# Kernel optimization log

Measured on AMD Instinct MI355X. Metric: run time of the kernel, lower is better.

## Reference

```python
import jax, jax.numpy as jnp
import numpy as np

NUM_AGENTS = 1000
N_ACTIONS = 16
HIDDEN = 256
COMM_STEPS = 4
B, M = 1024, 64


def setup_inputs() -> dict:
    key = jax.random.key(0)
    ks = jax.random.split(key, 8)
    agent_ids = jax.random.randint(ks[0], (B, M), 0, NUM_AGENTS)
    emb = jax.random.normal(ks[1], (NUM_AGENTS, HIDDEN), dtype=jnp.float32) * 0.1
    s1 = 1.0 / np.sqrt(3 * HIDDEN)
    W1 = jax.random.uniform(ks[2], (3 * HIDDEN, HIDDEN), jnp.float32, -s1, s1)
    b1 = jax.random.uniform(ks[3], (HIDDEN,), jnp.float32, -s1, s1)
    s2 = 1.0 / np.sqrt(HIDDEN)
    W2 = jax.random.uniform(ks[4], (HIDDEN, HIDDEN), jnp.float32, -s2, s2)
    b2 = jax.random.uniform(ks[5], (HIDDEN,), jnp.float32, -s2, s2)
    Wd = jax.random.uniform(ks[6], (HIDDEN, N_ACTIONS), jnp.float32, -s2, s2)
    bd = jax.random.uniform(ks[7], (N_ACTIONS,), jnp.float32, -s2, s2)
    return {"agent_ids": agent_ids, "emb": emb, "W1": W1, "b1": b1,
            "W2": W2, "b2": b2, "Wd": Wd, "bd": bd}


def reference(agent_ids, emb, W1, b1, W2, b2, Wd, bd):
    # h0: (B, M, H) embedding lookup
    h0 = emb[agent_ids]
    h = h0
    m = agent_ids.shape[1]
    inv = 1.0 / (m - 1)
    for _ in range(COMM_STEPS):
        # mean of other agents' hidden states: c_j = (sum_k h_k - h_j)/(M-1)
        c = (jnp.sum(h, axis=1, keepdims=True) - h) * inv
        x = jnp.concatenate([h, c, h0], axis=-1)  # (B, M, 3H)
        delta = jax.nn.relu(jnp.einsum('bmi,ih->bmh', x, W1) + b1)
        delta = jnp.einsum('bmi,ih->bmh', delta, W2) + b2
        h = h + delta  # residual (use_skip=True)
    logits = jnp.einsum('bmh,ha->bma', h, Wd) + bd
    return logits
```

## Files before the change

kernel.cpp:

```cpp
#include <hip/hip_runtime.h>

#define HID 256
#define NB 1024
#define NACT 16
#define HSTRIDE 528

typedef __bf16 bf16x8 __attribute__((ext_vector_type(8)));
typedef float  f32x4  __attribute__((ext_vector_type(4)));

#define HA_LO   33792
#define S_OFF   67584
#define LDS_TOT 68608

#define PREP_N (4 * 65536 + 4096)

__device__ __forceinline__ unsigned short f2bf(float x) {
    union { __bf16 b; unsigned short u; } v; v.b = (__bf16)x; return v.u;
}
__device__ __forceinline__ float bf2f(unsigned short u) {
    union { unsigned short u; __bf16 b; } v; v.u = u; return (float)v.b;
}
__device__ __forceinline__ float b2f_lo(unsigned v) { return bf2f((unsigned short)(v & 0xffffu)); }
__device__ __forceinline__ float b2f_hi(unsigned v) { return bf2f((unsigned short)(v >> 16)); }
__device__ __forceinline__ unsigned pack2(float a, float b) {
    return (unsigned)f2bf(a) | ((unsigned)f2bf(b) << 16);
}

__global__ __launch_bounds__(256) void prep_k(const float* __restrict__ W1,
                                              const float* __restrict__ W2,
                                              const float* __restrict__ Wd,
                                              unsigned short* __restrict__ WAh, unsigned short* __restrict__ WAl,
                                              unsigned short* __restrict__ WHh, unsigned short* __restrict__ WHl,
                                              unsigned short* __restrict__ WBh, unsigned short* __restrict__ WBl,
                                              unsigned short* __restrict__ WCh, unsigned short* __restrict__ WCl,
                                              unsigned short* __restrict__ WDh, unsigned short* __restrict__ WDl) {
    int i = blockIdx.x * 256 + threadIdx.x;
    const float inv = 1.0f / 63.0f;
    if (i < 4 * 65536) {
        int mat = i >> 16, j = i & 65535;
        int kq = j >> 13, r = j & 8191;
        int nb = r >> 9, r2 = r & 511;
        int l = r2 >> 3, e = r2 & 7;
        int n = nb * 16 + (l & 15);
        int k = kq * 32 + (l >> 4) * 8 + e;
        float val;
        if (mat == 0)      val = W1[k * 256 + n] - inv * W1[(256 + k) * 256 + n];
        else if (mat == 1) val = W1[(512 + k) * 256 + n];
        else if (mat == 2) val = W2[k * 256 + n];
        else               val = inv * W1[(256 + k) * 256 + n];
        unsigned short hi = f2bf(val);
        unsigned short lo = f2bf(val - bf2f(hi));
        if (mat == 0)      { WAh[j] = hi; WAl[j] = lo; }
        else if (mat == 1) { WHh[j] = hi; WHl[j] = lo; }
        else if (mat == 2) { WBh[j] = hi; WBl[j] = lo; }
        else               { WCh[j] = hi; WCl[j] = lo; }
    } else if (i < PREP_N) {
        int j = i - 4 * 65536, a = j >> 8, k = j & 255;
        float val = Wd[k * 16 + a];
        unsigned short hi = f2bf(val);
        WDh[j] = hi; WDl[j] = f2bf(val - bf2f(hi));
    }
}

__device__ __forceinline__ void kloopL2(const unsigned short* __restrict__ Wfh,
                                        const unsigned short* __restrict__ Wfl,
                                        const char* hA, f32x4 (&acc)[4][2],
                                        size_t lbase, int l15, int g)
{
    #pragma unroll 2
    for (int kq = 0; kq < 8; ++kq) {
        const int cb = g * 128 + kq * 16;
        bf16x8 ah[4], al[4];
        #pragma unroll
        for (int mt = 0; mt < 4; ++mt) {
            int rb = (mt * 16 + l15) * HSTRIDE;
            ah[mt] = *(const bf16x8*)(hA + rb + cb);
            al[mt] = *(const bf16x8*)(hA + HA_LO + rb + cb);
        }
        const size_t kb = (size_t)kq * 8192 + lbase;
        #pragma unroll
        for (int nt = 0; nt < 2; ++nt) {
            bf16x8 bh = *(const bf16x8*)(Wfh + kb + nt * 512);
            bf16x8 bl = *(const bf16x8*)(Wfl + kb + nt * 512);
            #pragma unroll
            for (int mt = 0; mt < 4; ++mt) {
                acc[mt][nt] = __builtin_amdgcn_mfma_f32_16x16x32_bf16(bh, ah[mt], acc[mt][nt], 0, 0, 0);
                acc[mt][nt] = __builtin_amdgcn_mfma_f32_16x16x32_bf16(bh, al[mt], acc[mt][nt], 0, 0, 0);
                acc[mt][nt] = __builtin_amdgcn_mfma_f32_16x16x32_bf16(bl, ah[mt], acc[mt][nt], 0, 0, 0);
            }
        }
    }
}

__global__ __launch_bounds__(512, 2) void fused_all(
    const int* __restrict__ ids, const float* __restrict__ emb,
    const unsigned short* __restrict__ WAh, const unsigned short* __restrict__ WAl,
    const unsigned short* __restrict__ WHh, const unsigned short* __restrict__ WHl,
    const unsigned short* __restrict__ WBh, const unsigned short* __restrict__ WBl,
    const unsigned short* __restrict__ WCh, const unsigned short* __restrict__ WCl,
    const unsigned short* __restrict__ WDh, const unsigned short* __restrict__ WDl,
    const float* __restrict__ b1, const float* __restrict__ b2,
    const float* __restrict__ bd, float* __restrict__ out)
{
    __shared__ __align__(16) char lds[LDS_TOT];
    const int tid = threadIdx.x;
    const int lane = tid & 63;
    const int w = tid >> 6;
    const int l15 = lane & 15, g = lane >> 4;
    const size_t rowbase = (size_t)blockIdx.x * 64;
    char* hA = lds;
    float* Sf = (float*)(lds + S_OFF);
    const size_t lbase = ((size_t)(w * 2) * 64 + lane) * 8;
    const int cb0 = w * 32 + g * 4;

    int colb[2];
    #pragma unroll
    for (int nt = 0; nt < 2; ++nt) {
        int o = w * 4 + nt * 2 + (g >> 1);
        colb[nt] = ((o & 3) * 8 + (o >> 2)) * 16 + (g & 1) * 8;
    }

    {
        int r = tid >> 3, c0q = tid & 7;
        const float4* src = (const float4*)(emb + (size_t)ids[rowbase + r] * HID + c0q * 32);
        char* dh = hA + r * HSTRIDE;
        #pragma unroll
        for (int j = 0; j < 8; ++j) {
            float4 v = src[j];
            unsigned short h0 = f2bf(v.x), h1 = f2bf(v.y), h2 = f2bf(v.z), h3 = f2bf(v.w);
            unsigned short q0 = f2bf(v.x - bf2f(h0)), q1 = f2bf(v.y - bf2f(h1)),
                           q2 = f2bf(v.z - bf2f(h2)), q3 = f2bf(v.w - bf2f(h3));
            int byte = (j >> 1) * 128 + c0q * 16 + (j & 1) * 8;
            *(uint2*)(dh + byte) = make_uint2((unsigned)h0 | ((unsigned)h1 << 16),
                                              (unsigned)h2 | ((unsigned)h3 << 16));
            *(uint2*)(dh + HA_LO + byte) = make_uint2((unsigned)q0 | ((unsigned)q1 << 16),
                                                      (unsigned)q2 | ((unsigned)q3 << 16));
        }
    }
    __syncthreads();

    if (tid < 256) {
        int cperm = (((tid >> 3) & 3) * 8 + (tid >> 5)) * 16 + (tid & 7) * 2;
        float ssum = 0.f;
        #pragma unroll 8
        for (int m = 0; m < 64; ++m) {
            int byte = m * HSTRIDE + cperm;
            ssum += bf2f(*(const unsigned short*)(hA + byte))
                  + bf2f(*(const unsigned short*)(hA + HA_LO + byte));
        }
        Sf[tid] = ssum;
    }
    __syncthreads();

    f32x4 acc[4][2], u0r[4][2];
    #pragma unroll
    for (int mt = 0; mt < 4; ++mt)
        #pragma unroll
        for (int nt = 0; nt < 2; ++nt) acc[mt][nt] = (f32x4){0.f, 0.f, 0.f, 0.f};

    kloopL2(WHh, WHl, hA, acc, lbase, l15, g);
    #pragma unroll
    for (int nt = 0; nt < 2; ++nt) {
        f32x4 b1v = *(const f32x4*)(b1 + cb0 + nt * 16);
        #pragma unroll
        for (int mt = 0; mt < 4; ++mt)
            u0r[mt][nt] = acc[mt][nt] + b1v;
    }

    for (int s = 0; s < 4; ++s) {
        f32x4 tacc[2];
        tacc[0] = tacc[1] = (f32x4){0.f, 0.f, 0.f, 0.f};
        #pragma unroll 2
        for (int kq = 0; kq < 8; ++kq) {
            const float* sp = Sf + kq * 32 + g * 8;
            f32x4 sa = *(const f32x4*)sp;
            f32x4 sb = *(const f32x4*)(sp + 4);
            unsigned sh[4], sl[4];
            sh[0] = pack2(sa[0], sa[1]); sh[1] = pack2(sa[2], sa[3]);
            sh[2] = pack2(sb[0], sb[1]); sh[3] = pack2(sb[2], sb[3]);
            sl[0] = pack2(sa[0] - b2f_lo(sh[0]), sa[1] - b2f_hi(sh[0]));
            sl[1] = pack2(sa[2] - b2f_lo(sh[1]), sa[3] - b2f_hi(sh[1]));
            sl[2] = pack2(sb[0] - b2f_lo(sh[2]), sb[1] - b2f_hi(sh[2]));
            sl[3] = pack2(sb[2] - b2f_lo(sh[3]), sb[3] - b2f_hi(sh[3]));
            bf16x8 shv = *(const bf16x8*)sh;
            bf16x8 slv = *(const bf16x8*)sl;
            const size_t kb = (size_t)kq * 8192 + lbase;
            #pragma unroll
            for (int nt = 0; nt < 2; ++nt) {
                bf16x8 wch = *(const bf16x8*)(WCh + kb + nt * 512);
                bf16x8 wcl = *(const bf16x8*)(WCl + kb + nt * 512);
                tacc[nt] = __builtin_amdgcn_mfma_f32_16x16x32_bf16(wch, shv, tacc[nt], 0, 0, 0);
                tacc[nt] = __builtin_amdgcn_mfma_f32_16x16x32_bf16(wch, slv, tacc[nt], 0, 0, 0);
                tacc[nt] = __builtin_amdgcn_mfma_f32_16x16x32_bf16(wcl, shv, tacc[nt], 0, 0, 0);
            }
        }

        #pragma unroll
        for (int mt = 0; mt < 4; ++mt)
            #pragma unroll
            for (int nt = 0; nt < 2; ++nt)
                acc[mt][nt] = u0r[mt][nt] + tacc[nt];
        kloopL2(WAh, WAl, hA, acc, lbase, l15, g);

        __syncthreads();
        #pragma unroll
        for (int mt = 0; mt < 4; ++mt)
            #pragma unroll
            for (int nt = 0; nt < 2; ++nt) {
                f32x4 b2v = *(const f32x4*)(b2 + cb0 + nt * 16);
                int byte = (mt * 16 + l15) * HSTRIDE + colb[nt];
                uint2 ph = *(const uint2*)(hA + byte);
                uint2 pl = *(const uint2*)(hA + HA_LO + byte);
                f32x4 hres;
                hres[0] = b2f_lo(ph.x) + b2f_lo(pl.x);
                hres[1] = b2f_hi(ph.x) + b2f_hi(pl.x);
                hres[2] = b2f_lo(ph.y) + b2f_lo(pl.y);
                hres[3] = b2f_hi(ph.y) + b2f_hi(pl.y);
                f32x4 av = acc[mt][nt];
                float a0 = fmaxf(av[0], 0.f), a1 = fmaxf(av[1], 0.f);
                float a2 = fmaxf(av[2], 0.f), a3 = fmaxf(av[3], 0.f);
                unsigned h01 = pack2(a0, a1), h23 = pack2(a2, a3);
                float r0 = a0 - b2f_lo(h01);
                float r1 = a1 - b2f_hi(h01);
                float r2 = a2 - b2f_lo(h23);
                float r3 = a3 - b2f_hi(h23);
                *(uint2*)(hA + byte) = make_uint2(h01, h23);
                *(uint2*)(hA + HA_LO + byte) = make_uint2(pack2(r0, r1), pack2(r2, r3));
                acc[mt][nt] = hres + b2v;
            }
        __syncthreads();

        kloopL2(WBh, WBl, hA, acc, lbase, l15, g);

        __syncthreads();
        #pragma unroll
        for (int mt = 0; mt < 4; ++mt)
            #pragma unroll
            for (int nt = 0; nt < 2; ++nt) {
                int byte = (mt * 16 + l15) * HSTRIDE + colb[nt];
                f32x4 av = acc[mt][nt];
                unsigned h01 = pack2(av[0], av[1]), h23 = pack2(av[2], av[3]);
                float r0 = av[0] - b2f_lo(h01);
                float r1 = av[1] - b2f_hi(h01);
                float r2 = av[2] - b2f_lo(h23);
                float r3 = av[3] - b2f_hi(h23);
                *(uint2*)(hA + byte) = make_uint2(h01, h23);
                *(uint2*)(hA + HA_LO + byte) = make_uint2(pack2(r0, r1), pack2(r2, r3));
            }
        if (s < 3) {
            #pragma unroll
            for (int nt = 0; nt < 2; ++nt) {
                f32x4 cs = (acc[0][nt] + acc[1][nt]) + (acc[2][nt] + acc[3][nt]);
                #pragma unroll
                for (int d = 1; d < 16; d <<= 1) {
                    cs[0] += __shfl_xor(cs[0], d);
                    cs[1] += __shfl_xor(cs[1], d);
                    cs[2] += __shfl_xor(cs[2], d);
                    cs[3] += __shfl_xor(cs[3], d);
                }
                if (l15 == 0) *(f32x4*)(Sf + cb0 + nt * 16) = cs;
            }
        }
        __syncthreads();
    }

    if (w < 4) {
        f32x4 dacc = (f32x4){0.f, 0.f, 0.f, 0.f};
        #pragma unroll 2
        for (int kq = 0; kq < 8; ++kq) {
            int byte = (w * 16 + l15) * HSTRIDE + g * 128 + kq * 16;
            bf16x8 hh = *(const bf16x8*)(hA + byte);
            bf16x8 hl = *(const bf16x8*)(hA + HA_LO + byte);
            const int k = kq * 32;
            bf16x8 wdh = *(const bf16x8*)(WDh + (size_t)l15 * 256 + k + g * 8);
            bf16x8 wdl = *(const bf16x8*)(WDl + (size_t)l15 * 256 + k + g * 8);
            dacc = __builtin_amdgcn_mfma_f32_16x16x32_bf16(wdh, hh, dacc, 0, 0, 0);
            dacc = __builtin_amdgcn_mfma_f32_16x16x32_bf16(wdh, hl, dacc, 0, 0, 0);
            dacc = __builtin_amdgcn_mfma_f32_16x16x32_bf16(wdl, hh, dacc, 0, 0, 0);
        }
        f32x4 bdv = *(const f32x4*)(bd + g * 4);
        f32x4 o = dacc + bdv;
        *(f32x4*)(out + (rowbase + w * 16 + l15) * NACT + g * 4) = o;
    }
}

extern "C" void kernel_launch(void* const* d_in, const int* in_sizes, int n_in,
                              void* d_out, int out_size, void* d_ws, size_t ws_size,
                              hipStream_t stream) {
    const int*   ids = (const int*)d_in[0];
    const float* emb = (const float*)d_in[1];
    const float* W1  = (const float*)d_in[2];
    const float* b1  = (const float*)d_in[3];
    const float* W2  = (const float*)d_in[4];
    const float* b2  = (const float*)d_in[5];
    const float* Wd  = (const float*)d_in[6];
    const float* bd  = (const float*)d_in[7];
    float* out = (float*)d_out;

    char* p = (char*)d_ws;
    unsigned short* WAh = (unsigned short*)p; p += 65536 * 2;
    unsigned short* WAl = (unsigned short*)p; p += 65536 * 2;
    unsigned short* WHh = (unsigned short*)p; p += 65536 * 2;
    unsigned short* WHl = (unsigned short*)p; p += 65536 * 2;
    unsigned short* WBh = (unsigned short*)p; p += 65536 * 2;
    unsigned short* WBl = (unsigned short*)p; p += 65536 * 2;
    unsigned short* WCh = (unsigned short*)p; p += 65536 * 2;
    unsigned short* WCl = (unsigned short*)p; p += 65536 * 2;
    unsigned short* WDh = (unsigned short*)p; p += 4096 * 2;
    unsigned short* WDl = (unsigned short*)p; p += 4096 * 2;

    prep_k<<<(PREP_N + 255) / 256, 256, 0, stream>>>(W1, W2, Wd, WAh, WAl, WHh, WHl,
                                                     WBh, WBl, WCh, WCl, WDh, WDl);
    fused_all<<<NB, 512, 0, stream>>>(ids, emb, WAh, WAl, WHh, WHl, WBh, WBl,
                                      WCh, WCl, WDh, WDl, b1, b2, bd, out);
}
```

Measured before the change: 278.4 us.

## Spill per-row h0 projection to global scratch and simplify LDS column layout

Moves the precomputed h0·W1 projection plus bias (u0r, 32 floats per lane) out of registers into a global workspace buffer, reloading it each communication step. The aim is to free VGPRs so the kernel can hold its launch bounds without spilling and improve occupancy. It also replaces the permuted column layout in LDS with a plain linear layout and changes the k-loop addressing to match. The cost is extra global memory traffic per step, and the new LDS access pattern may cause different bank conflicts.

Measured after the change: 352.5 us. 1.27x slower.

```diff
diff --git a/kernel.cpp b/kernel.cpp
--- a/kernel.cpp
+++ b/kernel.cpp
@@ -69,7 +69,7 @@
 {
     #pragma unroll 2
     for (int kq = 0; kq < 8; ++kq) {
-        const int cb = g * 128 + kq * 16;
+        const int cb = kq * 64 + g * 16;
         bf16x8 ah[4], al[4];
         #pragma unroll
         for (int mt = 0; mt < 4; ++mt) {
@@ -99,6 +99,7 @@
     const unsigned short* __restrict__ WBh, const unsigned short* __restrict__ WBl,
     const unsigned short* __restrict__ WCh, const unsigned short* __restrict__ WCl,
     const unsigned short* __restrict__ WDh, const unsigned short* __restrict__ WDl,
+    float* __restrict__ U0,
     const float* __restrict__ b1, const float* __restrict__ b2,
     const float* __restrict__ bd, float* __restrict__ out)
 {
@@ -112,39 +113,31 @@
     float* Sf = (float*)(lds + S_OFF);
     const size_t lbase = ((size_t)(w * 2) * 64 + lane) * 8;
     const int cb0 = w * 32 + g * 4;
-
-    int colb[2];
-    #pragma unroll
-    for (int nt = 0; nt < 2; ++nt) {
-        int o = w * 4 + nt * 2 + (g >> 1);
-        colb[nt] = ((o & 3) * 8 + (o >> 2)) * 16 + (g & 1) * 8;
-    }
+    f32x4* u0p = (f32x4*)U0 + (((size_t)blockIdx.x * 8 + w) * 8) * 64 + lane;
 
     {
-        int r = tid >> 3, c0q = tid & 7;
-        const float4* src = (const float4*)(emb + (size_t)ids[rowbase + r] * HID + c0q * 32);
-        char* dh = hA + r * HSTRIDE;
+        int r = tid >> 3, c0 = (tid & 7) * 32;
+        const float4* src = (const float4*)(emb + (size_t)ids[rowbase + r] * HID + c0);
+        char* dh = hA + r * HSTRIDE + c0 * 2;
         #pragma unroll
         for (int j = 0; j < 8; ++j) {
             float4 v = src[j];
             unsigned short h0 = f2bf(v.x), h1 = f2bf(v.y), h2 = f2bf(v.z), h3 = f2bf(v.w);
             unsigned short q0 = f2bf(v.x - bf2f(h0)), q1 = f2bf(v.y - bf2f(h1)),
                            q2 = f2bf(v.z - bf2f(h2)), q3 = f2bf(v.w - bf2f(h3));
-            int byte = (j >> 1) * 128 + c0q * 16 + (j & 1) * 8;
-            *(uint2*)(dh + byte) = make_uint2((unsigned)h0 | ((unsigned)h1 << 16),
-                                              (unsigned)h2 | ((unsigned)h3 << 16));
-            *(uint2*)(dh + HA_LO + byte) = make_uint2((unsigned)q0 | ((unsigned)q1 << 16),
-                                                      (unsigned)q2 | ((unsigned)q3 << 16));
+            *(uint2*)(dh + j * 8) = make_uint2((unsigned)h0 | ((unsigned)h1 << 16),
+                                               (unsigned)h2 | ((unsigned)h3 << 16));
+            *(uint2*)(dh + HA_LO + j * 8) = make_uint2((unsigned)q0 | ((unsigned)q1 << 16),
+                                                       (unsigned)q2 | ((unsigned)q3 << 16));
         }
     }
     __syncthreads();
 
     if (tid < 256) {
-        int cperm = (((tid >> 3) & 3) * 8 + (tid >> 5)) * 16 + (tid & 7) * 2;
         float ssum = 0.f;
         #pragma unroll 8
         for (int m = 0; m < 64; ++m) {
-            int byte = m * HSTRIDE + cperm;
+            int byte = m * HSTRIDE + tid * 2;
             ssum += bf2f(*(const unsigned short*)(hA + byte))
                   + bf2f(*(const unsigned short*)(hA + HA_LO + byte));
         }
@@ -152,7 +145,7 @@
     }
     __syncthreads();
 
-    f32x4 acc[4][2], u0r[4][2];
+    f32x4 acc[4][2];
     #pragma unroll
     for (int mt = 0; mt < 4; ++mt)
         #pragma unroll
@@ -163,8 +156,10 @@
     for (int nt = 0; nt < 2; ++nt) {
         f32x4 b1v = *(const f32x4*)(b1 + cb0 + nt * 16);
         #pragma unroll
-        for (int mt = 0; mt < 4; ++mt)
-            u0r[mt][nt] = acc[mt][nt] + b1v;
+        for (int mt = 0; mt < 4; ++mt) {
+            u0p[(mt * 2 + nt) * 64] = acc[mt][nt] + b1v;
+            acc[mt][nt] = (f32x4){0.f, 0.f, 0.f, 0.f};
+        }
     }
 
     for (int s = 0; s < 4; ++s) {
@@ -199,7 +194,7 @@
         for (int mt = 0; mt < 4; ++mt)
             #pragma unroll
             for (int nt = 0; nt < 2; ++nt)
-                acc[mt][nt] = u0r[mt][nt] + tacc[nt];
+                acc[mt][nt] = u0p[(mt * 2 + nt) * 64] + tacc[nt];
         kloopL2(WAh, WAl, hA, acc, lbase, l15, g);
 
         __syncthreads();
@@ -208,7 +203,7 @@
             #pragma unroll
             for (int nt = 0; nt < 2; ++nt) {
                 f32x4 b2v = *(const f32x4*)(b2 + cb0 + nt * 16);
-                int byte = (mt * 16 + l15) * HSTRIDE + colb[nt];
+                int byte = (mt * 16 + l15) * HSTRIDE + (cb0 + nt * 16) * 2;
                 uint2 ph = *(const uint2*)(hA + byte);
                 uint2 pl = *(const uint2*)(hA + HA_LO + byte);
                 f32x4 hres;
@@ -237,7 +232,7 @@
         for (int mt = 0; mt < 4; ++mt)
             #pragma unroll
             for (int nt = 0; nt < 2; ++nt) {
-                int byte = (mt * 16 + l15) * HSTRIDE + colb[nt];
+                int byte = (mt * 16 + l15) * HSTRIDE + (cb0 + nt * 16) * 2;
                 f32x4 av = acc[mt][nt];
                 unsigned h01 = pack2(av[0], av[1]), h23 = pack2(av[2], av[3]);
                 float r0 = av[0] - b2f_lo(h01);
@@ -268,7 +263,7 @@
         f32x4 dacc = (f32x4){0.f, 0.f, 0.f, 0.f};
         #pragma unroll 2
         for (int kq = 0; kq < 8; ++kq) {
-            int byte = (w * 16 + l15) * HSTRIDE + g * 128 + kq * 16;
+            int byte = (w * 16 + l15) * HSTRIDE + kq * 64 + g * 16;
             bf16x8 hh = *(const bf16x8*)(hA + byte);
             bf16x8 hl = *(const bf16x8*)(hA + HA_LO + byte);
             const int k = kq * 32;
@@ -308,9 +303,11 @@
     unsigned short* WCl = (unsigned short*)p; p += 65536 * 2;
     unsigned short* WDh = (unsigned short*)p; p += 4096 * 2;
     unsigned short* WDl = (unsigned short*)p; p += 4096 * 2;
+    p = (char*)(((uintptr_t)p + 255) & ~(uintptr_t)255);
+    float* U0 = (float*)p;
 
     prep_k<<<(PREP_N + 255) / 256, 256, 0, stream>>>(W1, W2, Wd, WAh, WAl, WHh, WHl,
                                                      WBh, WBl, WCh, WCl, WDh, WDl);
     fused_all<<<NB, 512, 0, stream>>>(ids, emb, WAh, WAl, WHh, WHl, WBh, WBl,
-                                      WCh, WCl, WDh, WDl, b1, b2, bd, out);
-}
+                                      WCh, WCl, WDh, WDl, U0, b1, b2, bd, out);
+}
```
